# Optimization experiments

Measured on AMD Instinct MI355X. Metric: run time of the kernel, lower is better.

The kernel has to match this reference:

```python
import jax, jax.numpy as jnp
import numpy as np

TOPK = 8
NUM_SEM = 32


def _forward(x, sem_w, sem_b, q_w, k_w, v_w, fuse_w, fuse_b, alpha, ln_gamma, ln_beta):
    B, C, H, W = x.shape
    N = H * W
    xf = x.reshape(B, C, N)

    # semantic soft-assignment (softmax over K regions per position)
    sem_logits = jnp.einsum('kc,bcn->bkn', sem_w, xf) + sem_b[None, :, None]
    sem = jax.nn.softmax(sem_logits, axis=1)
    sem = jnp.nan_to_num(sem, posinf=1e-6, neginf=0.0)

    # 1x1 conv projections as GEMMs
    q = jnp.einsum('dc,bcn->bdn', q_w, xf)   # (B,d,N)
    k = jnp.einsum('dc,bcn->bdn', k_w, xf)   # (B,d,N)
    v = jnp.einsum('oc,bcn->bon', v_w, xf)   # (B,C,N)
    d = q.shape[1]
    scale = d ** 0.5 + 1e-6

    # --- dense semantic-region attention branch ---
    region_k = jnp.einsum('bkn,bdn->bkd', sem, k)
    region_v = jnp.einsum('bkn,bcn->bkc', sem, v)
    attn_region = jax.nn.softmax(jnp.einsum('bdn,bkd->bkn', q, region_k) / scale, axis=1)
    attn_region = jnp.nan_to_num(attn_region, posinf=1e6, neginf=-1e6)
    cont_out = jnp.einsum('bkn,bkc->bcn', attn_region, region_v)
    cont_out = jnp.nan_to_num(cont_out, posinf=1e6, neginf=-1e6)

    # --- sparse top-k gather attention branch ---
    M = min(256, N)
    _, ti = jax.lax.top_k(jax.lax.stop_gradient(sem), M)       # (B,K,M) top positions per region
    hr = jnp.argmax(sem, axis=1)                                # (B,N) hard region per position
    idx_pp = jnp.take_along_axis(ti, hr[:, :, None], axis=1)    # (B,N,M) pool indices for each position

    bidx = jnp.arange(B)[:, None, None]
    qt = jnp.swapaxes(q, 1, 2)  # (B,N,d)
    kt = jnp.swapaxes(k, 1, 2)  # (B,N,d)
    vt = jnp.swapaxes(v, 1, 2)  # (B,N,C)

    kg = kt[bidx, idx_pp]                                       # (B,N,M,d) gathered key pool
    sims = jnp.einsum('bnd,bnmd->bnm', qt, kg) / scale          # (B,N,M)
    kn = min(TOPK, M)
    topv, topi = jax.lax.top_k(sims, kn)                        # (B,N,kn)
    att = jax.nn.softmax(topv, axis=-1)
    actual = jnp.take_along_axis(idx_pp, topi, axis=2)          # (B,N,kn) spatial indices
    vg = vt[bidx, actual]                                       # (B,N,kn,C)
    sparse_out = jnp.swapaxes(jnp.einsum('bnt,bntc->bnc', att, vg), 1, 2)  # (B,C,N)
    sparse_out = jnp.nan_to_num(sparse_out, posinf=1e6, neginf=-1e6)

    # --- combine, fuse, residual, channel LayerNorm ---
    a = jax.nn.sigmoid(alpha)
    combined = a * cont_out + (1.0 - a) * sparse_out
    combined = jnp.nan_to_num(combined, posinf=1e6, neginf=-1e6)
    fused = jnp.einsum('oc,bcn->bon', fuse_w, combined) + fuse_b[None, :, None]
    out = x + fused.reshape(B, C, H, W)

    xp = out.transpose(0, 2, 3, 1)  # (B,H,W,C)
    mu = xp.mean(-1, keepdims=True)
    var = xp.var(-1, keepdims=True)
    xp = (xp - mu) / jnp.sqrt(var + 1e-5) * ln_gamma + ln_beta
    return xp.transpose(0, 3, 1, 2)


def setup_inputs() -> dict:
    key = jax.random.key(0)
    ks = jax.random.split(key, 8)
    B, C, H, W = 2, 256, 64, 64
    d = C // 4  # reduction=4
    Ksem = NUM_SEM
    f32 = jnp.float32
    return {
        'x': jax.random.normal(ks[0], (B, C, H, W), f32),
        'sem_w': jax.random.normal(ks[1], (Ksem, C), f32) * 0.05,
        'sem_b': jnp.zeros((Ksem,), f32),
        'q_w': jax.random.normal(ks[2], (d, C), f32) * (2.0 / C) ** 0.5,
        'k_w': jax.random.normal(ks[3], (d, C), f32) * (2.0 / C) ** 0.5,
        'v_w': jax.random.normal(ks[4], (C, C), f32) * (2.0 / C) ** 0.5,
        'fuse_w': jax.random.normal(ks[5], (C, C), f32) * (1.0 / C) ** 0.5,
        'fuse_b': jnp.zeros((C,), f32),
        'alpha': jnp.float32(0.5),
        'ln_gamma': jnp.ones((C,), f32),
        'ln_beta': jnp.zeros((C,), f32),
    }


def reference(x, sem_w, sem_b, q_w, k_w, v_w, fuse_w, fuse_b, alpha, ln_gamma, ln_beta):
    return _forward(x, sem_w, sem_b, q_w, k_w, v_w, fuse_w, fuse_b, alpha, ln_gamma, ln_beta)
```

## Files before the change

kernel.cpp:

```cpp
#include <hip/hip_runtime.h>
#include <math.h>

#define QOFF 32
#define KOFF 96
#define VOFF 160
#define NSUB 8

__global__ __launch_bounds__(256) void proj_kernel(
    const float* __restrict__ x,
    const float* __restrict__ sem_w, const float* __restrict__ sem_b,
    const float* __restrict__ q_w, const float* __restrict__ k_w,
    const float* __restrict__ v_w, float* __restrict__ Y)
{
    const int t = threadIdx.x;
    const int n0 = blockIdx.x * 64;
    const int oc0 = blockIdx.y * 64;
    const int b = blockIdx.z;
    const int ty = t >> 4, tx = t & 15;

    __shared__ float As[16][68];
    __shared__ float Bs[16][64];

    float acc[4][4];
#pragma unroll
    for (int i = 0; i < 4; i++)
#pragma unroll
        for (int j = 0; j < 4; j++) acc[i][j] = 0.f;

    const int oc_l = t >> 2;
    const int cp = t & 3;
    const int oc_g = oc0 + oc_l;
    const float* wrow = nullptr;
    if (oc_g < 32) wrow = sem_w + oc_g * 256;
    else if (oc_g < 96) wrow = q_w + (oc_g - 32) * 256;
    else if (oc_g < 160) wrow = k_w + (oc_g - 96) * 256;
    else if (oc_g < 416) wrow = v_w + (oc_g - 160) * 256;

    const int bk = t >> 4;
    const int bn = (t & 15) << 2;

    for (int c0 = 0; c0 < 256; c0 += 16) {
        __syncthreads();
        float4 w4 = make_float4(0.f, 0.f, 0.f, 0.f);
        if (wrow) w4 = *(const float4*)(wrow + c0 + (cp << 2));
        As[(cp << 2) + 0][oc_l] = w4.x;
        As[(cp << 2) + 1][oc_l] = w4.y;
        As[(cp << 2) + 2][oc_l] = w4.z;
        As[(cp << 2) + 3][oc_l] = w4.w;
        *(float4*)&Bs[bk][bn] =
            *(const float4*)(x + ((size_t)(b * 256 + c0 + bk)) * 4096 + n0 + bn);
        __syncthreads();
#pragma unroll
        for (int kk = 0; kk < 16; kk++) {
            float4 a4 = *(float4*)&As[kk][ty << 2];
            float4 b4 = *(float4*)&Bs[kk][tx << 2];
            acc[0][0] += a4.x * b4.x; acc[0][1] += a4.x * b4.y;
            acc[0][2] += a4.x * b4.z; acc[0][3] += a4.x * b4.w;
            acc[1][0] += a4.y * b4.x; acc[1][1] += a4.y * b4.y;
            acc[1][2] += a4.y * b4.z; acc[1][3] += a4.y * b4.w;
            acc[2][0] += a4.z * b4.x; acc[2][1] += a4.z * b4.y;
            acc[2][2] += a4.z * b4.z; acc[2][3] += a4.z * b4.w;
            acc[3][0] += a4.w * b4.x; acc[3][1] += a4.w * b4.y;
            acc[3][2] += a4.w * b4.z; acc[3][3] += a4.w * b4.w;
        }
    }

    if (oc0 + (ty << 2) < 416) {
        float bias[4];
#pragma unroll
        for (int i = 0; i < 4; i++) {
            int oc = oc0 + (ty << 2) + i;
            bias[i] = (oc < 32) ? sem_b[oc] : 0.f;
        }
#pragma unroll
        for (int j = 0; j < 4; j++) {
            int n = n0 + (tx << 2) + j;
            float4 o4 = make_float4(acc[0][j] + bias[0], acc[1][j] + bias[1],
                                    acc[2][j] + bias[2], acc[3][j] + bias[3]);
            *(float4*)(Y + ((size_t)(b * 4096 + n)) * 416 + oc0 + (ty << 2)) = o4;
        }
    }
}

__global__ __launch_bounds__(256) void semsoft_kernel(float* __restrict__ Y,
                                                      int* __restrict__ hr)
{
    const int g = blockIdx.x * 256 + threadIdx.x;
    float* row = Y + (size_t)g * 416;
    float v[32];
#pragma unroll
    for (int i = 0; i < 8; i++) *(float4*)&v[i * 4] = *(float4*)&row[i * 4];
    float mx = v[0]; int am = 0;
#pragma unroll
    for (int kk = 1; kk < 32; kk++) if (v[kk] > mx) { mx = v[kk]; am = kk; }
    float s = 0.f;
#pragma unroll
    for (int kk = 0; kk < 32; kk++) { v[kk] = expf(v[kk] - mx); s += v[kk]; }
    const float inv = 1.f / s;
#pragma unroll
    for (int kk = 0; kk < 32; kk++) v[kk] *= inv;
#pragma unroll
    for (int i = 0; i < 8; i++) *(float4*)&row[i * 4] = *(float4*)&v[i * 4];
    hr[g] = am;
}

__global__ __launch_bounds__(256) void bin_kernel(
    const int* __restrict__ hr, int* __restrict__ cnt, int* __restrict__ plist)
{
    const int g = blockIdx.x * 256 + threadIdx.x;
    const int b = g >> 12, n = g & 4095;
    const int r = hr[g];
    const int slot = atomicAdd(&cnt[b * 32 + r], 1);
    plist[((size_t)(b * 32 + r)) * 4096 + slot] = n;
}

__global__ __launch_bounds__(256) void region_partial_kernel(
    const float* __restrict__ Y, float* __restrict__ P)
{
    const int ch = blockIdx.x, b = blockIdx.y;
    const int t = threadIdx.x;
    __shared__ float row_s[8][420];
    const int kset = t & 7;
    const int dds = t >> 3;
    float acc[4][10];
#pragma unroll
    for (int i = 0; i < 4; i++)
#pragma unroll
        for (int j = 0; j < 10; j++) acc[i][j] = 0.f;
    const size_t gbase = (size_t)(b * 4096 + ch * 128);
    for (int r0 = 0; r0 < 128; r0 += 8) {
        __syncthreads();
#pragma unroll
        for (int r = 0; r < 8; r++) {
            const float* rp = Y + (gbase + r0 + r) * 416;
            row_s[r][t] = rp[t];
            if (t < 160) row_s[r][t + 256] = rp[t + 256];
        }
        __syncthreads();
#pragma unroll
        for (int r = 0; r < 8; r++) {
            float sv[4], kv[10];
#pragma unroll
            for (int i = 0; i < 4; i++) sv[i] = row_s[r][(kset << 2) + i];
#pragma unroll
            for (int j = 0; j < 10; j++) kv[j] = row_s[r][96 + dds * 10 + j];
#pragma unroll
            for (int i = 0; i < 4; i++)
#pragma unroll
                for (int j = 0; j < 10; j++) acc[i][j] += sv[i] * kv[j];
        }
    }
    float* Pb = P + ((size_t)(b * 32 + ch)) * 10240;
#pragma unroll
    for (int i = 0; i < 4; i++)
#pragma unroll
        for (int j = 0; j < 10; j++)
            Pb[((kset << 2) + i) * 320 + dds * 10 + j] = acc[i][j];
}

__global__ __launch_bounds__(256) void region_reduce_kernel(
    const float* __restrict__ P, float* __restrict__ region)
{
    const int idx = blockIdx.x * 256 + threadIdx.x;
    if (idx >= 2 * 10240) return;
    const int b = idx / 10240, rem = idx - b * 10240;
    float s = 0.f;
    for (int ch = 0; ch < 32; ch++)
        s += P[((size_t)(b * 32 + ch)) * 10240 + rem];
    region[(size_t)b * 10240 + rem] = s;
}

__global__ __launch_bounds__(256) void topk_sem_kernel(
    const float* __restrict__ Y, int* __restrict__ ti)
{
    const int kreg = blockIdx.x, b = blockIdx.y;
    const int t = threadIdx.x;
    __shared__ int wpart[4];
    __shared__ int sh_eq[256];
    __shared__ int ctr;

    unsigned int uv[16];
    const int nbase = t * 16;
#pragma unroll
    for (int i = 0; i < 16; i++) {
        float v = Y[((size_t)(b * 4096 + nbase + i)) * 416 + kreg];
        unsigned int u = __float_as_uint(v);
        uv[i] = (u & 0x80000000u) ? ~u : (u | 0x80000000u);
    }
    unsigned long long lo = 0ull, hi = 0xFFFFFFFFull;
    while (lo < hi) {
        const unsigned int mid = (unsigned int)((lo + hi + 1ull) >> 1);
        int c = 0;
#pragma unroll
        for (int i = 0; i < 16; i++) c += (uv[i] >= mid) ? 1 : 0;
#pragma unroll
        for (int off = 1; off < 64; off <<= 1) c += __shfl_xor(c, off);
        __syncthreads();
        if ((t & 63) == 0) wpart[t >> 6] = c;
        __syncthreads();
        const int tot = wpart[0] + wpart[1] + wpart[2] + wpart[3];
        if (tot >= 256) lo = mid; else hi = (unsigned long long)mid - 1ull;
    }
    const unsigned int T = (unsigned int)lo;
    int cgt = 0, ceq = 0;
#pragma unroll
    for (int i = 0; i < 16; i++) { cgt += (uv[i] > T) ? 1 : 0; ceq += (uv[i] == T) ? 1 : 0; }
    int cg = cgt;
#pragma unroll
    for (int off = 1; off < 64; off <<= 1) cg += __shfl_xor(cg, off);
    __syncthreads();
    if ((t & 63) == 0) wpart[t >> 6] = cg;
    sh_eq[t] = ceq;
    if (t == 0) ctr = 0;
    __syncthreads();
    const int c1 = wpart[0] + wpart[1] + wpart[2] + wpart[3];
    int eqbase = 0;
    for (int i = 0; i < t; i++) eqbase += sh_eq[i];
    int* outp = ti + ((size_t)(b * 32 + kreg)) * 256;
    int seen = 0;
#pragma unroll
    for (int i = 0; i < 16; i++) {
        if (uv[i] > T) {
            int pos = atomicAdd(&ctr, 1);
            outp[pos] = nbase + i;
        } else if (uv[i] == T) {
            int r = eqbase + seen; seen++;
            if (c1 + r < 256) outp[c1 + r] = nbase + i;
        }
    }
}

__global__ __launch_bounds__(256) void sparse_attn_kernel(
    const float* __restrict__ Y, const int* __restrict__ cnt,
    const int* __restrict__ plist, const int* __restrict__ ti,
    float* __restrict__ sp)
{
    const int rb = blockIdx.x;
    const int sub = blockIdx.y;
    const int b = rb >> 5;
    const int t = threadIdx.x, wid = t >> 6, lane = t & 63;

    const int count = cnt[rb];
    const int chunk = (count + NSUB - 1) / NSUB;
    const int p0 = sub * chunk;
    const int p1 = min(p0 + chunk, count);
    if (p1 <= p0) return;
    const int npass = (p1 - p0 + 15) >> 4;

    __shared__ int pool_s[256];
    __shared__ float K_sT[64][128];
    __shared__ float q_sT[4][64][4];
    __shared__ float sims_s[4][4][256];

    if (t < 64)
        *(int4*)&pool_s[t << 2] = *(const int4*)(ti + (size_t)rb * 256 + (t << 2));
    __syncthreads();

    const float inv_scale = 1.0f / (8.0f + 1e-6f);
    const int* myplist = plist + (size_t)rb * 4096;
    const int krow = t >> 1;
    const int jh = t & 1;

    for (int pass = 0; pass < npass; pass++) {
        int gg[4]; bool val[4];
#pragma unroll
        for (int p = 0; p < 4; p++) {
            const int idx = p0 + (pass << 4) + (wid << 2) + p;
            val[p] = (idx < p1);
            const int n = myplist[val[p] ? idx : p0];
            gg[p] = (b << 12) + n;
            q_sT[wid][lane][p] = Y[(size_t)gg[p] * 416 + QOFF + lane];
        }

        for (int half = 0; half < 2; half++) {
            __syncthreads();
            {
                const int kidx = pool_s[(half << 7) + krow];
                const float* kr = Y + ((size_t)((b << 12) + kidx)) * 416 + KOFF + (jh << 5);
#pragma unroll
                for (int jj = 0; jj < 8; jj++) {
                    float4 kv = *(const float4*)(kr + (jj << 2));
                    const int jb = (jh << 5) + (jj << 2);
                    K_sT[jb + 0][krow] = kv.x;
                    K_sT[jb + 1][krow] = kv.y;
                    K_sT[jb + 2][krow] = kv.z;
                    K_sT[jb + 3][krow] = kv.w;
                }
            }
            __syncthreads();
            float a00 = 0.f, a01 = 0.f, a10 = 0.f, a11 = 0.f;
            float a20 = 0.f, a21 = 0.f, a30 = 0.f, a31 = 0.f;
#pragma unroll
            for (int j = 0; j < 64; j++) {
                const float2 kv = *(const float2*)&K_sT[j][lane << 1];
                const float4 q4 = *(const float4*)&q_sT[wid][j][0];
                a00 += q4.x * kv.x; a01 += q4.x * kv.y;
                a10 += q4.y * kv.x; a11 += q4.y * kv.y;
                a20 += q4.z * kv.x; a21 += q4.z * kv.y;
                a30 += q4.w * kv.x; a31 += q4.w * kv.y;
            }
            const int sbase = (half << 7) + (lane << 1);
            *(float2*)&sims_s[wid][0][sbase] = make_float2(a00 * inv_scale, a01 * inv_scale);
            *(float2*)&sims_s[wid][1][sbase] = make_float2(a10 * inv_scale, a11 * inv_scale);
            *(float2*)&sims_s[wid][2][sbase] = make_float2(a20 * inv_scale, a21 * inv_scale);
            *(float2*)&sims_s[wid][3][sbase] = make_float2(a30 * inv_scale, a31 * inv_scale);
        }
        asm volatile("s_waitcnt lgkmcnt(0)" ::: "memory");

#pragma unroll
        for (int p = 0; p < 4; p++) {
            if (!val[p]) continue;
            float4 sv = *(const float4*)&sims_s[wid][p][lane << 2];
            float s0 = sv.x, s1 = sv.y, s2 = sv.z, s3 = sv.w;
            float topv[8]; int topm[8];
#pragma unroll
            for (int sel = 0; sel < 8; sel++) {
                float bv = s0; int bm = (lane << 2);
                if (s1 > bv) { bv = s1; bm = (lane << 2) + 1; }
                if (s2 > bv) { bv = s2; bm = (lane << 2) + 2; }
                if (s3 > bv) { bv = s3; bm = (lane << 2) + 3; }
#pragma unroll
                for (int off = 1; off < 64; off <<= 1) {
                    const float ov = __shfl_xor(bv, off);
                    const int om = __shfl_xor(bm, off);
                    if (ov > bv || (ov == bv && om < bm)) { bv = ov; bm = om; }
                }
                topv[sel] = bv; topm[sel] = bm;
                const bool own = (lane == (bm >> 2));
                const int sl = bm & 3;
                s0 = (own && sl == 0) ? -3e38f : s0;
                s1 = (own && sl == 1) ? -3e38f : s1;
                s2 = (own && sl == 2) ? -3e38f : s2;
                s3 = (own && sl == 3) ? -3e38f : s3;
            }
            const float mx = topv[0];
            float att[8]; float esum = 0.f;
#pragma unroll
            for (int j = 0; j < 8; j++) { att[j] = expf(topv[j] - mx); esum += att[j]; }
            const float inv = 1.f / esum;
            float4 acc = make_float4(0.f, 0.f, 0.f, 0.f);
#pragma unroll
            for (int j = 0; j < 8; j++) {
                const int actual = pool_s[topm[j]];
                const float4 vv = *(const float4*)(
                    Y + ((size_t)((b << 12) + actual)) * 416 + VOFF + (lane << 2));
                const float w = att[j] * inv;
                acc.x += w * vv.x; acc.y += w * vv.y;
                acc.z += w * vv.z; acc.w += w * vv.w;
            }
            *(float4*)(sp + (size_t)gg[p] * 256 + (lane << 2)) = acc;
        }
    }
}

__global__ __launch_bounds__(256) void combine_kernel(
    const float* __restrict__ Y, const float* __restrict__ region,
    const float* __restrict__ alpha, float* __restrict__ sp)
{
    const int t = threadIdx.x, wid = t >> 6, lane = t & 63;
    const int b = blockIdx.y;
    const int n0 = blockIdx.x << 5;
    __shared__ float rk_s[32][65];
    __shared__ float rv_s[32][256];
    __shared__ float q_all[32][64];

    const float* reg = region + (size_t)b * 10240;
    for (int idx = t; idx < 10240; idx += 256) {
        const int kk = idx / 320, dd = idx - kk * 320;
        const float v = reg[idx];
        if (dd < 64) rk_s[kk][dd] = v; else rv_s[kk][dd - 64] = v;
    }
    const size_t g0 = (size_t)(b << 12) + n0;
    for (int idx = t; idx < 2048; idx += 256)
        q_all[idx >> 6][idx & 63] = Y[(g0 + (idx >> 6)) * 416 + QOFF + (idx & 63)];
    __syncthreads();

    const float asig = 1.f / (1.f + expf(-alpha[0]));
    const float inv_scale = 1.0f / (8.0f + 1e-6f);
    const int kk = lane & 31, half = lane >> 5;

    for (int pp = 0; pp < 8; pp++) {
        const int n_l = (wid << 3) + pp;
        const size_t g = g0 + n_l;
        float part = 0.f;
        {
            const float* qr = &q_all[n_l][half << 5];
            const float* rkr = &rk_s[kk][half << 5];
#pragma unroll
            for (int j = 0; j < 32; j++) part += qr[j] * rkr[j];
        }
        part += __shfl_xor(part, 32);
        const float logit = part * inv_scale;
        float mx = logit;
#pragma unroll
        for (int off = 1; off < 32; off <<= 1) mx = fmaxf(mx, __shfl_xor(mx, off));
        const float e = expf(logit - mx);
        float s = e;
#pragma unroll
        for (int off = 1; off < 32; off <<= 1) s += __shfl_xor(s, off);
        const float w_own = e / s;

        float4 acc = make_float4(0.f, 0.f, 0.f, 0.f);
#pragma unroll
        for (int k2 = 0; k2 < 32; k2++) {
            const float w = __shfl(w_own, k2);
            const float4 rv = *(const float4*)&rv_s[k2][lane << 2];
            acc.x += w * rv.x; acc.y += w * rv.y;
            acc.z += w * rv.z; acc.w += w * rv.w;
        }
        float* spr = sp + g * 256 + (lane << 2);
        float4 spv = *(float4*)spr;
        float4 o;
        o.x = asig * acc.x + (1.f - asig) * spv.x;
        o.y = asig * acc.y + (1.f - asig) * spv.y;
        o.z = asig * acc.z + (1.f - asig) * spv.z;
        o.w = asig * acc.w + (1.f - asig) * spv.w;
        *(float4*)spr = o;
    }
}

__global__ __launch_bounds__(256) void fuse_ln_kernel(
    const float* __restrict__ comb, const float* __restrict__ fuse_w,
    const float* __restrict__ fuse_b, const float* __restrict__ x,
    const float* __restrict__ ln_g, const float* __restrict__ ln_b,
    float* __restrict__ out)
{
    const int t = threadIdx.x;
    const int n0 = blockIdx.x << 5;
    const int b = blockIdx.y;

    __shared__ float smem[32 * 256 + 32 * 36];
    float (*Ws)[256] = (float (*)[256])smem;
    float (*cs)[36] = (float (*)[36])(smem + 32 * 256);
    float (*Fs)[260] = (float (*)[260])smem;
    __shared__ float red1[8][32], red2[8][32];
    __shared__ float mu_s[32], rs_s[32];

    const int og = t & 63;
    const int ng = t >> 6;
    float acc[4][8];
#pragma unroll
    for (int i = 0; i < 4; i++)
#pragma unroll
        for (int j = 0; j < 8; j++) acc[i][j] = 0.f;

    const int cl = (t << 2) & 31;
    const int nl = t >> 3;

    for (int c0 = 0; c0 < 256; c0 += 32) {
        __syncthreads();
        {
            const float* wr = fuse_w + (size_t)t * 256 + c0;
#pragma unroll
            for (int j = 0; j < 8; j++) {
                float4 w4 = *(const float4*)(wr + (j << 2));
                Ws[(j << 2) + 0][t] = w4.x;
                Ws[(j << 2) + 1][t] = w4.y;
                Ws[(j << 2) + 2][t] = w4.z;
                Ws[(j << 2) + 3][t] = w4.w;
            }
        }
        {
            float4 c4 = *(const float4*)(
                comb + ((size_t)(b * 4096 + n0 + nl)) * 256 + c0 + cl);
            cs[cl + 0][nl] = c4.x;
            cs[cl + 1][nl] = c4.y;
            cs[cl + 2][nl] = c4.z;
            cs[cl + 3][nl] = c4.w;
        }
        __syncthreads();
#pragma unroll
        for (int cc = 0; cc < 32; cc++) {
            float4 w4 = *(float4*)&Ws[cc][og << 2];
            float4 ca = *(float4*)&cs[cc][ng << 3];
            float4 cb = *(float4*)&cs[cc][(ng << 3) + 4];
            float wv[4] = {w4.x, w4.y, w4.z, w4.w};
            float cv[8] = {ca.x, ca.y, ca.z, ca.w, cb.x, cb.y, cb.z, cb.w};
#pragma unroll
            for (int i = 0; i < 4; i++)
#pragma unroll
                for (int j = 0; j < 8; j++) acc[i][j] += wv[i] * cv[j];
        }
    }

    __syncthreads();
#pragma unroll
    for (int i = 0; i < 4; i++) {
        const int o = (og << 2) + i;
        const float fb = fuse_b[o];
        const float* xr = x + ((size_t)(b * 256 + o)) * 4096 + n0 + (ng << 3);
        float4 xa = *(const float4*)xr;
        float4 xb = *(const float4*)(xr + 4);
        float xv[8] = {xa.x, xa.y, xa.z, xa.w, xb.x, xb.y, xb.z, xb.w};
#pragma unroll
        for (int j = 0; j < 8; j++)
            Fs[(ng << 3) + j][o] = acc[i][j] + fb + xv[j];
    }
    __syncthreads();
    {
        const int n = t & 31, part = t >> 5;
        float s1 = 0.f, s2 = 0.f;
#pragma unroll
        for (int i = 0; i < 32; i++) {
            const float v = Fs[n][(part << 5) + i];
            s1 += v; s2 += v * v;
        }
        red1[part][n] = s1; red2[part][n] = s2;
    }
    __syncthreads();
    if (t < 32) {
        float s1 = 0.f, s2 = 0.f;
#pragma unroll
        for (int p = 0; p < 8; p++) { s1 += red1[p][t]; s2 += red2[p][t]; }
        const float mean = s1 * (1.f / 256.f);
        const float var = s2 * (1.f / 256.f) - mean * mean;
        mu_s[t] = mean;
        rs_s[t] = rsqrtf(var + 1e-5f);
    }
    __syncthreads();
#pragma unroll
    for (int j = 0; j < 32; j++) {
        const int idx = (j << 8) + t;
        const int o = idx >> 5, n = idx & 31;
        const float v = (Fs[n][o] - mu_s[n]) * rs_s[n] * ln_g[o] + ln_b[o];
        out[((size_t)(b * 256 + o)) * 4096 + n0 + n] = v;
    }
}

extern "C" void kernel_launch(void* const* d_in, const int* in_sizes, int n_in,
                              void* d_out, int out_size, void* d_ws, size_t ws_size,
                              hipStream_t stream)
{
    const float* x = (const float*)d_in[0];
    const float* sem_w = (const float*)d_in[1];
    const float* sem_b = (const float*)d_in[2];
    const float* q_w = (const float*)d_in[3];
    const float* k_w = (const float*)d_in[4];
    const float* v_w = (const float*)d_in[5];
    const float* fuse_w = (const float*)d_in[6];
    const float* fuse_b = (const float*)d_in[7];
    const float* alpha = (const float*)d_in[8];
    const float* ln_g = (const float*)d_in[9];
    const float* ln_b = (const float*)d_in[10];
    float* out = (float*)d_out;

    char* ws = (char*)d_ws;
    float* Y    = (float*)(ws);
    float* SP   = (float*)(ws + 13631488);
    float* P    = (float*)(ws + 22020096);
    float* REG  = (float*)(ws + 24641536);
    int*   HR   = (int*)  (ws + 24723456);
    int*   TI   = (int*)  (ws + 24756224);
    int*   CNT  = (int*)  (ws + 24821760);
    int*   PLIST= (int*)  (ws + 24822016);

    proj_kernel<<<dim3(64, 7, 2), 256, 0, stream>>>(x, sem_w, sem_b, q_w, k_w, v_w, Y);
    semsoft_kernel<<<32, 256, 0, stream>>>(Y, HR);
    hipMemsetAsync(CNT, 0, 256, stream);
    bin_kernel<<<32, 256, 0, stream>>>(HR, CNT, PLIST);
    region_partial_kernel<<<dim3(32, 2), 256, 0, stream>>>(Y, P);
    region_reduce_kernel<<<80, 256, 0, stream>>>(P, REG);
    topk_sem_kernel<<<dim3(32, 2), 256, 0, stream>>>(Y, TI);
    sparse_attn_kernel<<<dim3(64, NSUB), 256, 0, stream>>>(Y, CNT, PLIST, TI, SP);
    combine_kernel<<<dim3(128, 2), 256, 0, stream>>>(Y, REG, alpha, SP);
    fuse_ln_kernel<<<dim3(128, 2), 256, 0, stream>>>(SP, fuse_w, fuse_b, x, ln_g, ln_b, out);
}
```

Before: 331.6 us.

## Preload full key pool once in sparse attention and split region partials across column groups

The sparse attention kernel now gathers all 256 pooled key rows into shared memory once per block, instead of regathering them on every pass. The scores are kept in registers instead of being written to a shared sims buffer, which removes per-pass barriers and repeated global gathers. The region partial kernel gains a third grid dimension of 5 column groups of 64, each computing a 32x64 tile, so it launches 320 blocks instead of 64 and uses more of the GPU. The trade-off is 64KB of shared memory for the key pool, which may reduce occupancy.

```diff
diff --git a/kernel.cpp b/kernel.cpp
--- a/kernel.cpp
+++ b/kernel.cpp
@@ -117,45 +117,50 @@
 __global__ __launch_bounds__(256) void region_partial_kernel(
     const float* __restrict__ Y, float* __restrict__ P)
 {
-    const int ch = blockIdx.x, b = blockIdx.y;
+    const int ch = blockIdx.x;
+    const int b  = blockIdx.y;
+    const int dg = blockIdx.z;
     const int t = threadIdx.x;
-    __shared__ float row_s[8][420];
-    const int kset = t & 7;
-    const int dds = t >> 3;
-    float acc[4][10];
-#pragma unroll
-    for (int i = 0; i < 4; i++)
-#pragma unroll
-        for (int j = 0; j < 10; j++) acc[i][j] = 0.f;
+    __shared__ float sem_s[16][33];
+    __shared__ float kv_s[16][68];
+    const int kg = t >> 4;
+    const int dq = t & 15;
+    float acc[2][4];
+#pragma unroll
+    for (int i = 0; i < 2; i++)
+#pragma unroll
+        for (int j = 0; j < 4; j++) acc[i][j] = 0.f;
+
     const size_t gbase = (size_t)(b * 4096 + ch * 128);
-    for (int r0 = 0; r0 < 128; r0 += 8) {
-        __syncthreads();
-#pragma unroll
-        for (int r = 0; r < 8; r++) {
-            const float* rp = Y + (gbase + r0 + r) * 416;
-            row_s[r][t] = rp[t];
-            if (t < 160) row_s[r][t + 256] = rp[t + 256];
-        }
-        __syncthreads();
-#pragma unroll
-        for (int r = 0; r < 8; r++) {
-            float sv[4], kv[10];
-#pragma unroll
-            for (int i = 0; i < 4; i++) sv[i] = row_s[r][(kset << 2) + i];
-#pragma unroll
-            for (int j = 0; j < 10; j++) kv[j] = row_s[r][96 + dds * 10 + j];
-#pragma unroll
-            for (int i = 0; i < 4; i++)
-#pragma unroll
-                for (int j = 0; j < 10; j++) acc[i][j] += sv[i] * kv[j];
-        }
-    }
-    float* Pb = P + ((size_t)(b * 32 + ch)) * 10240;
-#pragma unroll
-    for (int i = 0; i < 4; i++)
-#pragma unroll
-        for (int j = 0; j < 10; j++)
-            Pb[((kset << 2) + i) * 320 + dds * 10 + j] = acc[i][j];
+    const int sr = t >> 4, sc = (t & 15) << 2;
+    for (int r0 = 0; r0 < 128; r0 += 16) {
+        __syncthreads();
+        {
+            sem_s[t >> 5][t & 31] = Y[(gbase + r0 + (t >> 5)) * 416 + (t & 31)];
+            const int i2 = t + 256;
+            sem_s[i2 >> 5][i2 & 31] = Y[(gbase + r0 + (i2 >> 5)) * 416 + (i2 & 31)];
+        }
+        {
+            *(float4*)&kv_s[sr][sc] =
+                *(const float4*)(Y + (gbase + r0 + sr) * 416 + 96 + dg * 64 + sc);
+        }
+        __syncthreads();
+#pragma unroll
+        for (int r = 0; r < 16; r++) {
+            const float s0 = sem_s[r][(kg << 1) + 0];
+            const float s1 = sem_s[r][(kg << 1) + 1];
+            const float4 kv = *(float4*)&kv_s[r][dq << 2];
+            acc[0][0] += s0 * kv.x; acc[0][1] += s0 * kv.y;
+            acc[0][2] += s0 * kv.z; acc[0][3] += s0 * kv.w;
+            acc[1][0] += s1 * kv.x; acc[1][1] += s1 * kv.y;
+            acc[1][2] += s1 * kv.z; acc[1][3] += s1 * kv.w;
+        }
+    }
+    float* Pb = P + ((size_t)(b * 32 + ch)) * 10240 + dg * 64;
+#pragma unroll
+    for (int i = 0; i < 2; i++)
+        *(float4*)&Pb[((kg << 1) + i) * 320 + (dq << 2)] =
+            make_float4(acc[i][0], acc[i][1], acc[i][2], acc[i][3]);
 }
 
 __global__ __launch_bounds__(256) void region_reduce_kernel(
@@ -240,7 +245,8 @@
     const int b = rb >> 5;
     const int t = threadIdx.x, wid = t >> 6, lane = t & 63;
 
-    const int count = cnt[rb];
+    int count = cnt[rb];
+    count = min(max(count, 0), 4096);
     const int chunk = (count + NSUB - 1) / NSUB;
     const int p0 = sub * chunk;
     const int p1 = min(p0 + chunk, count);
@@ -248,18 +254,34 @@
     const int npass = (p1 - p0 + 15) >> 4;
 
     __shared__ int pool_s[256];
-    __shared__ float K_sT[64][128];
+    __shared__ float K_sT[64][256];
     __shared__ float q_sT[4][64][4];
-    __shared__ float sims_s[4][4][256];
 
     if (t < 64)
         *(int4*)&pool_s[t << 2] = *(const int4*)(ti + (size_t)rb * 256 + (t << 2));
     __syncthreads();
+    {
+        const int krow = t >> 1, jh = t & 1;
+#pragma unroll
+        for (int hh = 0; hh < 2; hh++) {
+            const int key = (hh << 7) + krow;
+            const int kidx = pool_s[key];
+            const float* kr = Y + ((size_t)((b << 12) + kidx)) * 416 + KOFF + (jh << 5);
+#pragma unroll
+            for (int jj = 0; jj < 8; jj++) {
+                float4 kv = *(const float4*)(kr + (jj << 2));
+                const int jb = (jh << 5) + (jj << 2);
+                K_sT[jb + 0][key] = kv.x;
+                K_sT[jb + 1][key] = kv.y;
+                K_sT[jb + 2][key] = kv.z;
+                K_sT[jb + 3][key] = kv.w;
+            }
+        }
+    }
+    __syncthreads();
 
     const float inv_scale = 1.0f / (8.0f + 1e-6f);
     const int* myplist = plist + (size_t)rb * 4096;
-    const int krow = t >> 1;
-    const int jh = t & 1;
 
     for (int pass = 0; pass < npass; pass++) {
         int gg[4]; bool val[4];
@@ -271,54 +293,41 @@
             gg[p] = (b << 12) + n;
             q_sT[wid][lane][p] = Y[(size_t)gg[p] * 416 + QOFF + lane];
         }
-
-        for (int half = 0; half < 2; half++) {
-            __syncthreads();
-            {
-                const int kidx = pool_s[(half << 7) + krow];
-                const float* kr = Y + ((size_t)((b << 12) + kidx)) * 416 + KOFF + (jh << 5);
-#pragma unroll
-                for (int jj = 0; jj < 8; jj++) {
-                    float4 kv = *(const float4*)(kr + (jj << 2));
-                    const int jb = (jh << 5) + (jj << 2);
-                    K_sT[jb + 0][krow] = kv.x;
-                    K_sT[jb + 1][krow] = kv.y;
-                    K_sT[jb + 2][krow] = kv.z;
-                    K_sT[jb + 3][krow] = kv.w;
-                }
-            }
-            __syncthreads();
-            float a00 = 0.f, a01 = 0.f, a10 = 0.f, a11 = 0.f;
-            float a20 = 0.f, a21 = 0.f, a30 = 0.f, a31 = 0.f;
-#pragma unroll
-            for (int j = 0; j < 64; j++) {
-                const float2 kv = *(const float2*)&K_sT[j][lane << 1];
-                const float4 q4 = *(const float4*)&q_sT[wid][j][0];
-                a00 += q4.x * kv.x; a01 += q4.x * kv.y;
-                a10 += q4.y * kv.x; a11 += q4.y * kv.y;
-                a20 += q4.z * kv.x; a21 += q4.z * kv.y;
-                a30 += q4.w * kv.x; a31 += q4.w * kv.y;
-            }
-            const int sbase = (half << 7) + (lane << 1);
-            *(float2*)&sims_s[wid][0][sbase] = make_float2(a00 * inv_scale, a01 * inv_scale);
-            *(float2*)&sims_s[wid][1][sbase] = make_float2(a10 * inv_scale, a11 * inv_scale);
-            *(float2*)&sims_s[wid][2][sbase] = make_float2(a20 * inv_scale, a21 * inv_scale);
-            *(float2*)&sims_s[wid][3][sbase] = make_float2(a30 * inv_scale, a31 * inv_scale);
-        }
         asm volatile("s_waitcnt lgkmcnt(0)" ::: "memory");
+
+        float a[4][4];
+#pragma unroll
+        for (int p = 0; p < 4; p++)
+#pragma unroll
+            for (int sl = 0; sl < 4; sl++) a[p][sl] = 0.f;
+#pragma unroll
+        for (int j = 0; j < 64; j++) {
+            const float2 k0 = *(const float2*)&K_sT[j][lane << 1];
+            const float2 k1 = *(const float2*)&K_sT[j][128 + (lane << 1)];
+            const float4 q4 = *(const float4*)&q_sT[wid][j][0];
+            a[0][0] += q4.x * k0.x; a[0][1] += q4.x * k0.y;
+            a[0][2] += q4.x * k1.x; a[0][3] += q4.x * k1.y;
+            a[1][0] += q4.y * k0.x; a[1][1] += q4.y * k0.y;
+            a[1][2] += q4.y * k1.x; a[1][3] += q4.y * k1.y;
+            a[2][0] += q4.z * k0.x; a[2][1] += q4.z * k0.y;
+            a[2][2] += q4.z * k1.x; a[2][3] += q4.z * k1.y;
+            a[3][0] += q4.w * k0.x; a[3][1] += q4.w * k0.y;
+            a[3][2] += q4.w * k1.x; a[3][3] += q4.w * k1.y;
+        }
 
 #pragma unroll
         for (int p = 0; p < 4; p++) {
             if (!val[p]) continue;
-            float4 sv = *(const float4*)&sims_s[wid][p][lane << 2];
-            float s0 = sv.x, s1 = sv.y, s2 = sv.z, s3 = sv.w;
+            float s0 = a[p][0] * inv_scale, s1 = a[p][1] * inv_scale;
+            float s2 = a[p][2] * inv_scale, s3 = a[p][3] * inv_scale;
+            const int m0 = lane << 1;
             float topv[8]; int topm[8];
 #pragma unroll
             for (int sel = 0; sel < 8; sel++) {
-                float bv = s0; int bm = (lane << 2);
-                if (s1 > bv) { bv = s1; bm = (lane << 2) + 1; }
-                if (s2 > bv) { bv = s2; bm = (lane << 2) + 2; }
-                if (s3 > bv) { bv = s3; bm = (lane << 2) + 3; }
+                float bv = s0; int bm = m0;
+                if (s1 > bv) { bv = s1; bm = m0 + 1; }
+                if (s2 > bv) { bv = s2; bm = 128 + m0; }
+                if (s3 > bv) { bv = s3; bm = 128 + m0 + 1; }
 #pragma unroll
                 for (int off = 1; off < 64; off <<= 1) {
                     const float ov = __shfl_xor(bv, off);
@@ -326,12 +335,14 @@
                     if (ov > bv || (ov == bv && om < bm)) { bv = ov; bm = om; }
                 }
                 topv[sel] = bv; topm[sel] = bm;
-                const bool own = (lane == (bm >> 2));
-                const int sl = bm & 3;
-                s0 = (own && sl == 0) ? -3e38f : s0;
-                s1 = (own && sl == 1) ? -3e38f : s1;
-                s2 = (own && sl == 2) ? -3e38f : s2;
-                s3 = (own && sl == 3) ? -3e38f : s3;
+                const int owner = (bm & 127) >> 1;
+                const int sl = (bm & 1) | ((bm >> 7) << 1);
+                if (lane == owner) {
+                    s0 = (sl == 0) ? -3e38f : s0;
+                    s1 = (sl == 1) ? -3e38f : s1;
+                    s2 = (sl == 2) ? -3e38f : s2;
+                    s3 = (sl == 3) ? -3e38f : s3;
+                }
             }
             const float mx = topv[0];
             float att[8]; float esum = 0.f;
@@ -558,7 +569,7 @@
     semsoft_kernel<<<32, 256, 0, stream>>>(Y, HR);
     hipMemsetAsync(CNT, 0, 256, stream);
     bin_kernel<<<32, 256, 0, stream>>>(HR, CNT, PLIST);
-    region_partial_kernel<<<dim3(32, 2), 256, 0, stream>>>(Y, P);
+    region_partial_kernel<<<dim3(32, 2, 5), 256, 0, stream>>>(Y, P);
     region_reduce_kernel<<<80, 256, 0, stream>>>(P, REG);
     topk_sem_kernel<<<dim3(32, 2), 256, 0, stream>>>(Y, TI);
     sparse_attn_kernel<<<dim3(64, NSUB), 256, 0, stream>>>(Y, CNT, PLIST, TI, SP);
```

Result: no change. 329.4 us (-0.6%).
